# Performance work log

Hardware: AMD Instinct MI355X
Metric: run time of the kernel (lower is better)

The kernel has to match this reference:

```python
import jax, jax.numpy as jnp
import numpy as np

N = 50000   # nodes
E = 800000  # edges
H = 128     # hidden dim
V = 50000   # feats_per_node (embedding vocab)


def setup_inputs() -> dict:
    key = jax.random.key(0)
    ks = jax.random.split(key, 16)
    s = 0.05  # keep activations in a sane range
    return {
        "node_ids": jax.random.randint(ks[0], (N,), 0, V),
        "src": jax.random.randint(ks[1], (E,), 0, N),
        "dst": jnp.sort(jax.random.randint(ks[2], (E,), 0, N)),
        "emb": jax.random.normal(ks[3], (V, H), jnp.float32) * s,
        "W_pool1": jax.random.normal(ks[4], (H, H), jnp.float32) * s,
        "b_pool1": jax.random.normal(ks[5], (H,), jnp.float32) * s,
        "W_self1": jax.random.normal(ks[6], (H, H), jnp.float32) * s,
        "W_neigh1": jax.random.normal(ks[7], (H, H), jnp.float32) * s,
        "b1": jax.random.normal(ks[8], (H,), jnp.float32) * s,
        "W_pool2": jax.random.normal(ks[9], (H, H), jnp.float32) * s,
        "b_pool2": jax.random.normal(ks[10], (H,), jnp.float32) * s,
        "W_self2": jax.random.normal(ks[11], (H, H), jnp.float32) * s,
        "W_neigh2": jax.random.normal(ks[12], (H, H), jnp.float32) * s,
        "b2": jax.random.normal(ks[13], (H,), jnp.float32) * s,
    }


def _sage_pool_layer(h, src, dst, W_pool, b_pool, W_self, W_neigh, b):
    # DGL SAGEConv('pool'): per-src MLP, gather over edges, segmented max per dst.
    m = jax.nn.relu(h @ W_pool + b_pool)              # [N, H]
    msgs = m[src]                                     # [E, H] gather
    agg = jax.ops.segment_max(msgs, dst, num_segments=N,
                              indices_are_sorted=True)  # [N, H]
    agg = jnp.where(jnp.isneginf(agg), 0.0, agg)      # zero-in-degree -> 0 (DGL semantics)
    return h @ W_self + agg @ W_neigh + b


def reference(node_ids, src, dst, emb,
              W_pool1, b_pool1, W_self1, W_neigh1, b1,
              W_pool2, b_pool2, W_self2, W_neigh2, b2):
    h = emb[node_ids]                                 # embedding_h on 1-hot indices
    h = _sage_pool_layer(h, src, dst, W_pool1, b_pool1, W_self1, W_neigh1, b1)
    h = _sage_pool_layer(h, src, dst, W_pool2, b_pool2, W_self2, W_neigh2, b2)
    return h
```

## Files before the change

### kernel.cpp

```cpp
#include <hip/hip_runtime.h>

#define HD 128

typedef __attribute__((ext_vector_type(8))) short short8;
typedef __attribute__((ext_vector_type(4))) float floatx4;

typedef unsigned short ushort_t;
typedef unsigned int uint_t;

__device__ __forceinline__ ushort_t f2b(float f) {
    union { float f; uint_t u; } v; v.f = f;
    uint_t r = v.u + 0x7fff + ((v.u >> 16) & 1);
    return (ushort_t)(r >> 16);
}
__device__ __forceinline__ float b_lo(uint_t p) {
    union { uint_t u; float f; } v; v.u = p << 16; return v.f;
}
__device__ __forceinline__ float b_hi(uint_t p) {
    union { uint_t u; float f; } v; v.u = p & 0xffff0000u; return v.f;
}
__device__ __forceinline__ uint_t packb(float a, float b) {
    union { float f; uint_t u; } x, y; x.f = a; y.f = b;
    return (x.u >> 16) | (y.u & 0xffff0000u);
}

__global__ __launch_bounds__(256) void k_prep(const int* __restrict__ dst, int E,
                                              int* __restrict__ rp, int N,
                                              const int* __restrict__ ids,
                                              const float* __restrict__ emb,
                                              ushort_t* __restrict__ h0,
                                              const float* W0, const float* W1,
                                              const float* W2, const float* W3,
                                              const float* W4, const float* W5,
                                              ushort_t* __restrict__ Wpk,
                                              int nbG, int nbR) {
    int b = blockIdx.x;
    if (b < nbG) {
        int idx = b * 256 + threadIdx.x;
        int row = idx >> 5;
        if (row >= N) return;
        int c = (idx & 31) * 4;
        float4 v = *(const float4*)&emb[(size_t)ids[row] * HD + c];
        uint2 o;
        o.x = (uint_t)f2b(v.x) | ((uint_t)f2b(v.y) << 16);
        o.y = (uint_t)f2b(v.z) | ((uint_t)f2b(v.w) << 16);
        *(uint2*)&h0[(size_t)row * HD + c] = o;
    } else if (b < nbG + nbR) {
        int i = (b - nbG) * 256 + threadIdx.x;
        if (i > N) return;
        int lo = 0, hi = E;
        while (lo < hi) {
            int mid = (lo + hi) >> 1;
            if (dst[mid] < i) lo = mid + 1; else hi = mid;
        }
        rp[i] = lo;
    } else {
        int bb = b - nbG - nbR;
        const float* Ws[6] = {W0, W1, W2, W3, W4, W5};
        int mat = bb >> 6;
        int o = ((bb & 63) << 8) + threadIdx.x;
        int j = o & 7, l = (o >> 3) & 63, s = (o >> 9) & 3, t = o >> 11;
        int k = s * 32 + ((l >> 4) & 3) * 8 + j;
        int n = t * 16 + (l & 15);
        Wpk[(size_t)mat * 16384 + o] = f2b(Ws[mat][k * HD + n]);
    }
}

__global__ __launch_bounds__(256) void k_pool_mfma(const ushort_t* __restrict__ h,
                                                   const ushort_t* __restrict__ Wpk,
                                                   const float* __restrict__ bias,
                                                   ushort_t* __restrict__ m, int N) {
    int wave = blockIdx.x * 4 + (threadIdx.x >> 6);
    int row0 = wave * 32;
    if (row0 >= N) return;
    int l = threadIdx.x & 63;
    int ar0 = row0 + (l & 15); if (ar0 >= N) ar0 = N - 1;
    int ar1 = ar0 + 16;        if (ar1 >= N) ar1 = N - 1;
    int ac = (l >> 4) * 8;
    short8 a0[4], a1[4];
#pragma unroll
    for (int s = 0; s < 4; ++s) {
        a0[s] = *(const short8*)&h[(size_t)ar0 * HD + s * 32 + ac];
        a1[s] = *(const short8*)&h[(size_t)ar1 * HD + s * 32 + ac];
    }
    int rb = row0 + (l >> 4) * 4;
#pragma unroll
    for (int t = 0; t < 8; ++t) {
        floatx4 acc0 = {0.f, 0.f, 0.f, 0.f};
        floatx4 acc1 = {0.f, 0.f, 0.f, 0.f};
#pragma unroll
        for (int s = 0; s < 4; ++s) {
            short8 b = *(const short8*)&Wpk[(t * 4 + s) * 512 + l * 8];
            acc0 = __builtin_amdgcn_mfma_f32_16x16x32_bf16(a0[s], b, acc0, 0, 0, 0);
            acc1 = __builtin_amdgcn_mfma_f32_16x16x32_bf16(a1[s], b, acc1, 0, 0, 0);
        }
        int col = t * 16 + (l & 15);
        float bv = bias[col];
#pragma unroll
        for (int r = 0; r < 4; ++r) {
            int g0 = rb + r, g1 = rb + 16 + r;
            if (g0 < N) m[(size_t)g0 * HD + col] = f2b(fmaxf(acc0[r] + bv, 0.f));
            if (g1 < N) m[(size_t)g1 * HD + col] = f2b(fmaxf(acc1[r] + bv, 0.f));
        }
    }
}

template <bool F32OUT>
__global__ __launch_bounds__(256) void k_dual_mfma(const ushort_t* __restrict__ h,
                                                   const ushort_t* __restrict__ agg,
                                                   const ushort_t* __restrict__ WsPk,
                                                   const ushort_t* __restrict__ WnPk,
                                                   const float* __restrict__ bias,
                                                   void* __restrict__ outp, int N) {
    int wave = blockIdx.x * 4 + (threadIdx.x >> 6);
    int row0 = wave * 32;
    if (row0 >= N) return;
    int l = threadIdx.x & 63;
    int ar0 = row0 + (l & 15); if (ar0 >= N) ar0 = N - 1;
    int ar1 = ar0 + 16;        if (ar1 >= N) ar1 = N - 1;
    int ac = (l >> 4) * 8;
    short8 ah0[4], ah1[4], ag0[4], ag1[4];
#pragma unroll
    for (int s = 0; s < 4; ++s) {
        ah0[s] = *(const short8*)&h[(size_t)ar0 * HD + s * 32 + ac];
        ah1[s] = *(const short8*)&h[(size_t)ar1 * HD + s * 32 + ac];
        ag0[s] = *(const short8*)&agg[(size_t)ar0 * HD + s * 32 + ac];
        ag1[s] = *(const short8*)&agg[(size_t)ar1 * HD + s * 32 + ac];
    }
    int rb = row0 + (l >> 4) * 4;
#pragma unroll
    for (int t = 0; t < 8; ++t) {
        floatx4 acc0 = {0.f, 0.f, 0.f, 0.f};
        floatx4 acc1 = {0.f, 0.f, 0.f, 0.f};
#pragma unroll
        for (int s = 0; s < 4; ++s) {
            short8 bs = *(const short8*)&WsPk[(t * 4 + s) * 512 + l * 8];
            acc0 = __builtin_amdgcn_mfma_f32_16x16x32_bf16(ah0[s], bs, acc0, 0, 0, 0);
            acc1 = __builtin_amdgcn_mfma_f32_16x16x32_bf16(ah1[s], bs, acc1, 0, 0, 0);
        }
#pragma unroll
        for (int s = 0; s < 4; ++s) {
            short8 bn = *(const short8*)&WnPk[(t * 4 + s) * 512 + l * 8];
            acc0 = __builtin_amdgcn_mfma_f32_16x16x32_bf16(ag0[s], bn, acc0, 0, 0, 0);
            acc1 = __builtin_amdgcn_mfma_f32_16x16x32_bf16(ag1[s], bn, acc1, 0, 0, 0);
        }
        int col = t * 16 + (l & 15);
        float bv = bias[col];
#pragma unroll
        for (int r = 0; r < 4; ++r) {
            int g0 = rb + r, g1 = rb + 16 + r;
            float v0 = acc0[r] + bv, v1 = acc1[r] + bv;
            if (F32OUT) {
                if (g0 < N) ((float*)outp)[(size_t)g0 * HD + col] = v0;
                if (g1 < N) ((float*)outp)[(size_t)g1 * HD + col] = v1;
            } else {
                if (g0 < N) ((ushort_t*)outp)[(size_t)g0 * HD + col] = f2b(v0);
                if (g1 < N) ((ushort_t*)outp)[(size_t)g1 * HD + col] = f2b(v1);
            }
        }
    }
}

__global__ __launch_bounds__(256) void k_segmax(const ushort_t* __restrict__ m,
                                                const int* __restrict__ src,
                                                const int* __restrict__ rp,
                                                ushort_t* __restrict__ agg, int N) {
    int node = blockIdx.x * 8 + (threadIdx.x >> 5);
    if (node >= N) return;
    int lane = threadIdx.x & 31;
    int beg = rp[node], end = rp[node + 1];
    float a0 = 0.f, a1 = 0.f, a2 = 0.f, a3 = 0.f;
    float c0 = 0.f, c1 = 0.f, c2 = 0.f, c3 = 0.f;
    int e = beg;
    int e4 = beg + ((end - beg) & ~3);
    for (; e < e4; e += 4) {
        int s0 = src[e], s1 = src[e + 1], s2 = src[e + 2], s3 = src[e + 3];
        uint2 p0 = *(const uint2*)&m[(size_t)s0 * HD + lane * 4];
        uint2 p1 = *(const uint2*)&m[(size_t)s1 * HD + lane * 4];
        uint2 p2 = *(const uint2*)&m[(size_t)s2 * HD + lane * 4];
        uint2 p3 = *(const uint2*)&m[(size_t)s3 * HD + lane * 4];
        a0 = fmaxf(a0, b_lo(p0.x)); a1 = fmaxf(a1, b_hi(p0.x));
        a2 = fmaxf(a2, b_lo(p0.y)); a3 = fmaxf(a3, b_hi(p0.y));
        c0 = fmaxf(c0, b_lo(p1.x)); c1 = fmaxf(c1, b_hi(p1.x));
        c2 = fmaxf(c2, b_lo(p1.y)); c3 = fmaxf(c3, b_hi(p1.y));
        a0 = fmaxf(a0, b_lo(p2.x)); a1 = fmaxf(a1, b_hi(p2.x));
        a2 = fmaxf(a2, b_lo(p2.y)); a3 = fmaxf(a3, b_hi(p2.y));
        c0 = fmaxf(c0, b_lo(p3.x)); c1 = fmaxf(c1, b_hi(p3.x));
        c2 = fmaxf(c2, b_lo(p3.y)); c3 = fmaxf(c3, b_hi(p3.y));
    }
    for (; e < end; ++e) {
        uint2 p = *(const uint2*)&m[(size_t)src[e] * HD + lane * 4];
        a0 = fmaxf(a0, b_lo(p.x)); a1 = fmaxf(a1, b_hi(p.x));
        a2 = fmaxf(a2, b_lo(p.y)); a3 = fmaxf(a3, b_hi(p.y));
    }
    a0 = fmaxf(a0, c0); a1 = fmaxf(a1, c1); a2 = fmaxf(a2, c2); a3 = fmaxf(a3, c3);
    uint2 o; o.x = packb(a0, a1); o.y = packb(a2, a3);
    *(uint2*)&agg[(size_t)node * HD + lane * 4] = o;
}

extern "C" void kernel_launch(void* const* d_in, const int* in_sizes, int n_in,
                              void* d_out, int out_size, void* d_ws, size_t ws_size,
                              hipStream_t stream) {
    const int*   node_ids = (const int*)d_in[0];
    const int*   src      = (const int*)d_in[1];
    const int*   dst      = (const int*)d_in[2];
    const float* emb      = (const float*)d_in[3];
    const float* Wp1      = (const float*)d_in[4];
    const float* bp1      = (const float*)d_in[5];
    const float* Ws1      = (const float*)d_in[6];
    const float* Wn1      = (const float*)d_in[7];
    const float* b1       = (const float*)d_in[8];
    const float* Wp2      = (const float*)d_in[9];
    const float* bp2      = (const float*)d_in[10];
    const float* Ws2      = (const float*)d_in[11];
    const float* Wn2      = (const float*)d_in[12];
    const float* b2       = (const float*)d_in[13];
    float* out = (float*)d_out;

    const int N = in_sizes[0];
    const int E = in_sizes[1];

    char* ws = (char*)d_ws;
    int* rp = (int*)ws;
    size_t off = (((size_t)(N + 1) * 4) + 255) & ~(size_t)255;
    ushort_t* Wpk  = (ushort_t*)(ws + off);
    ushort_t* h0   = Wpk + 6 * 16384;
    ushort_t* bufM = h0 + (size_t)N * HD;
    ushort_t* bufA = bufM + (size_t)N * HD;
    ushort_t* h1   = bufA + (size_t)N * HD;

    const int nbG = (N * 32 + 255) / 256;
    const int nbR = (N + 1 + 255) / 256;
    const int nbP = 6 * 64;
    const int nb_gemm = (N + 127) / 128;
    const int nb_seg  = (N + 7) / 8;

    k_prep<<<nbG + nbR + nbP, 256, 0, stream>>>(dst, E, rp, N, node_ids, emb, h0,
                                                Wp1, Ws1, Wn1, Wp2, Ws2, Wn2, Wpk,
                                                nbG, nbR);

    const ushort_t* Wp1k = Wpk;
    const ushort_t* Ws1k = Wpk + 16384;
    const ushort_t* Wn1k = Wpk + 2 * 16384;
    const ushort_t* Wp2k = Wpk + 3 * 16384;
    const ushort_t* Ws2k = Wpk + 4 * 16384;
    const ushort_t* Wn2k = Wpk + 5 * 16384;

    k_pool_mfma<<<nb_gemm, 256, 0, stream>>>(h0, Wp1k, bp1, bufM, N);
    k_segmax<<<nb_seg, 256, 0, stream>>>(bufM, src, rp, bufA, N);
    k_dual_mfma<false><<<nb_gemm, 256, 0, stream>>>(h0, bufA, Ws1k, Wn1k, b1, h1, N);

    k_pool_mfma<<<nb_gemm, 256, 0, stream>>>(h1, Wp2k, bp2, bufM, N);
    k_segmax<<<nb_seg, 256, 0, stream>>>(bufM, src, rp, bufA, N);
    k_dual_mfma<true><<<nb_gemm, 256, 0, stream>>>(h1, bufA, Ws2k, Wn2k, b2, out, N);
}
```

Before: 245.9 us.

## Fuse embedding gather into first pool GEMM, stage weights in LDS, widen segmax

The embedding gather and bf16 conversion move out of the prep kernel and into the first pool GEMM, which writes h0 as a side output. All GEMM kernels now copy their packed weights into shared memory once per block instead of reading them from global memory on every wave. Segmax now assigns a full 64-lane wave per node, with the two half-waves taking alternate edges and merging through a cross-lane shuffle. The price is 32-64 KB of LDS per GEMM block, which may lower occupancy, plus extra staging work in every block.

```diff
diff --git a/kernel.cpp b/kernel.cpp
--- a/kernel.cpp
+++ b/kernel.cpp
@@ -23,30 +23,23 @@
     union { float f; uint_t u; } x, y; x.f = a; y.f = b;
     return (x.u >> 16) | (y.u & 0xffff0000u);
 }
+__device__ __forceinline__ short8 cvt8(const float* __restrict__ p) {
+    float4 u = *(const float4*)p, v = *(const float4*)(p + 4);
+    short8 r;
+    r[0] = (short)f2b(u.x); r[1] = (short)f2b(u.y); r[2] = (short)f2b(u.z); r[3] = (short)f2b(u.w);
+    r[4] = (short)f2b(v.x); r[5] = (short)f2b(v.y); r[6] = (short)f2b(v.z); r[7] = (short)f2b(v.w);
+    return r;
+}
 
 __global__ __launch_bounds__(256) void k_prep(const int* __restrict__ dst, int E,
                                               int* __restrict__ rp, int N,
-                                              const int* __restrict__ ids,
-                                              const float* __restrict__ emb,
-                                              ushort_t* __restrict__ h0,
                                               const float* W0, const float* W1,
                                               const float* W2, const float* W3,
                                               const float* W4, const float* W5,
-                                              ushort_t* __restrict__ Wpk,
-                                              int nbG, int nbR) {
+                                              ushort_t* __restrict__ Wpk, int nbR) {
     int b = blockIdx.x;
-    if (b < nbG) {
-        int idx = b * 256 + threadIdx.x;
-        int row = idx >> 5;
-        if (row >= N) return;
-        int c = (idx & 31) * 4;
-        float4 v = *(const float4*)&emb[(size_t)ids[row] * HD + c];
-        uint2 o;
-        o.x = (uint_t)f2b(v.x) | ((uint_t)f2b(v.y) << 16);
-        o.y = (uint_t)f2b(v.z) | ((uint_t)f2b(v.w) << 16);
-        *(uint2*)&h0[(size_t)row * HD + c] = o;
-    } else if (b < nbG + nbR) {
-        int i = (b - nbG) * 256 + threadIdx.x;
+    if (b < nbR) {
+        int i = b * 256 + threadIdx.x;
         if (i > N) return;
         int lo = 0, hi = E;
         while (lo < hi) {
@@ -55,7 +48,7 @@
         }
         rp[i] = lo;
     } else {
-        int bb = b - nbG - nbR;
+        int bb = b - nbR;
         const float* Ws[6] = {W0, W1, W2, W3, W4, W5};
         int mat = bb >> 6;
         int o = ((bb & 63) << 8) + threadIdx.x;
@@ -66,10 +59,71 @@
     }
 }
 
-__global__ __launch_bounds__(256) void k_pool_mfma(const ushort_t* __restrict__ h,
-                                                   const ushort_t* __restrict__ Wpk,
-                                                   const float* __restrict__ bias,
-                                                   ushort_t* __restrict__ m, int N) {
+__device__ __forceinline__ void stage_w(const ushort_t* __restrict__ g,
+                                        ushort_t* l, int tid) {
+#pragma unroll
+    for (int i = 0; i < 8; ++i) {
+        int off = i * 2048 + tid * 8;
+        *(short8*)&l[off] = *(const short8*)&g[off];
+    }
+}
+
+__global__ __launch_bounds__(256) void k_gather_pool(const int* __restrict__ ids,
+                                                     const float* __restrict__ emb,
+                                                     const ushort_t* __restrict__ Wpk,
+                                                     const float* __restrict__ bias,
+                                                     ushort_t* __restrict__ h0,
+                                                     ushort_t* __restrict__ m, int N) {
+    __shared__ ushort_t Wl[16384];
+    stage_w(Wpk, Wl, threadIdx.x);
+    __syncthreads();
+
+    int wave = blockIdx.x * 4 + (threadIdx.x >> 6);
+    int row0 = wave * 32;
+    if (row0 >= N) return;
+    int l = threadIdx.x & 63;
+    int ar0 = row0 + (l & 15); if (ar0 >= N) ar0 = N - 1;
+    int ar1 = ar0 + 16;        if (ar1 >= N) ar1 = N - 1;
+    int ac = (l >> 4) * 8;
+    int id0 = ids[ar0], id1 = ids[ar1];
+    short8 a0[4], a1[4];
+#pragma unroll
+    for (int s = 0; s < 4; ++s) {
+        a0[s] = cvt8(&emb[(size_t)id0 * HD + s * 32 + ac]);
+        a1[s] = cvt8(&emb[(size_t)id1 * HD + s * 32 + ac]);
+        *(short8*)&h0[(size_t)ar0 * HD + s * 32 + ac] = a0[s];
+        *(short8*)&h0[(size_t)ar1 * HD + s * 32 + ac] = a1[s];
+    }
+    int rb = row0 + (l >> 4) * 4;
+#pragma unroll
+    for (int t = 0; t < 8; ++t) {
+        floatx4 acc0 = {0.f, 0.f, 0.f, 0.f};
+        floatx4 acc1 = {0.f, 0.f, 0.f, 0.f};
+#pragma unroll
+        for (int s = 0; s < 4; ++s) {
+            short8 b = *(const short8*)&Wl[(t * 4 + s) * 512 + l * 8];
+            acc0 = __builtin_amdgcn_mfma_f32_16x16x32_bf16(a0[s], b, acc0, 0, 0, 0);
+            acc1 = __builtin_amdgcn_mfma_f32_16x16x32_bf16(a1[s], b, acc1, 0, 0, 0);
+        }
+        int col = t * 16 + (l & 15);
+        float bv = bias[col];
+#pragma unroll
+        for (int r = 0; r < 4; ++r) {
+            int g0 = rb + r, g1 = rb + 16 + r;
+            if (g0 < N) m[(size_t)g0 * HD + col] = f2b(fmaxf(acc0[r] + bv, 0.f));
+            if (g1 < N) m[(size_t)g1 * HD + col] = f2b(fmaxf(acc1[r] + bv, 0.f));
+        }
+    }
+}
+
+__global__ __launch_bounds__(256) void k_pool(const ushort_t* __restrict__ h,
+                                              const ushort_t* __restrict__ Wpk,
+                                              const float* __restrict__ bias,
+                                              ushort_t* __restrict__ m, int N) {
+    __shared__ ushort_t Wl[16384];
+    stage_w(Wpk, Wl, threadIdx.x);
+    __syncthreads();
+
     int wave = blockIdx.x * 4 + (threadIdx.x >> 6);
     int row0 = wave * 32;
     if (row0 >= N) return;
@@ -90,7 +144,7 @@
         floatx4 acc1 = {0.f, 0.f, 0.f, 0.f};
 #pragma unroll
         for (int s = 0; s < 4; ++s) {
-            short8 b = *(const short8*)&Wpk[(t * 4 + s) * 512 + l * 8];
+            short8 b = *(const short8*)&Wl[(t * 4 + s) * 512 + l * 8];
             acc0 = __builtin_amdgcn_mfma_f32_16x16x32_bf16(a0[s], b, acc0, 0, 0, 0);
             acc1 = __builtin_amdgcn_mfma_f32_16x16x32_bf16(a1[s], b, acc1, 0, 0, 0);
         }
@@ -105,13 +159,63 @@
     }
 }
 
+__global__ __launch_bounds__(256) void k_segmax(const ushort_t* __restrict__ m,
+                                                const int* __restrict__ src,
+                                                const int* __restrict__ rp,
+                                                ushort_t* __restrict__ agg, int N) {
+    int node = blockIdx.x * 4 + (threadIdx.x >> 6);
+    if (node >= N) return;
+    int l = threadIdx.x & 63;
+    int half = l >> 5;
+    int col4 = (l & 31) * 4;
+    int beg = rp[node], end = rp[node + 1];
+    float a0 = 0.f, a1 = 0.f, a2 = 0.f, a3 = 0.f;
+    float c0 = 0.f, c1 = 0.f, c2 = 0.f, c3 = 0.f;
+    int e = beg;
+    for (; e + 8 <= end; e += 8) {
+        int e0 = e + half, e1 = e + 2 + half, e2 = e + 4 + half, e3 = e + 6 + half;
+        uint2 p0 = *(const uint2*)&m[(size_t)src[e0] * HD + col4];
+        uint2 p1 = *(const uint2*)&m[(size_t)src[e1] * HD + col4];
+        uint2 p2 = *(const uint2*)&m[(size_t)src[e2] * HD + col4];
+        uint2 p3 = *(const uint2*)&m[(size_t)src[e3] * HD + col4];
+        a0 = fmaxf(a0, b_lo(p0.x)); a1 = fmaxf(a1, b_hi(p0.x));
+        a2 = fmaxf(a2, b_lo(p0.y)); a3 = fmaxf(a3, b_hi(p0.y));
+        c0 = fmaxf(c0, b_lo(p1.x)); c1 = fmaxf(c1, b_hi(p1.x));
+        c2 = fmaxf(c2, b_lo(p1.y)); c3 = fmaxf(c3, b_hi(p1.y));
+        a0 = fmaxf(a0, b_lo(p2.x)); a1 = fmaxf(a1, b_hi(p2.x));
+        a2 = fmaxf(a2, b_lo(p2.y)); a3 = fmaxf(a3, b_hi(p2.y));
+        c0 = fmaxf(c0, b_lo(p3.x)); c1 = fmaxf(c1, b_hi(p3.x));
+        c2 = fmaxf(c2, b_lo(p3.y)); c3 = fmaxf(c3, b_hi(p3.y));
+    }
+    for (; e < end; e += 2) {
+        int ee = e + half; if (ee >= end) ee = end - 1;
+        uint2 p = *(const uint2*)&m[(size_t)src[ee] * HD + col4];
+        a0 = fmaxf(a0, b_lo(p.x)); a1 = fmaxf(a1, b_hi(p.x));
+        a2 = fmaxf(a2, b_lo(p.y)); a3 = fmaxf(a3, b_hi(p.y));
+    }
+    a0 = fmaxf(a0, c0); a1 = fmaxf(a1, c1); a2 = fmaxf(a2, c2); a3 = fmaxf(a3, c3);
+    a0 = fmaxf(a0, __shfl_xor(a0, 32));
+    a1 = fmaxf(a1, __shfl_xor(a1, 32));
+    a2 = fmaxf(a2, __shfl_xor(a2, 32));
+    a3 = fmaxf(a3, __shfl_xor(a3, 32));
+    if (half == 0) {
+        uint2 o; o.x = packb(a0, a1); o.y = packb(a2, a3);
+        *(uint2*)&agg[(size_t)node * HD + col4] = o;
+    }
+}
+
 template <bool F32OUT>
-__global__ __launch_bounds__(256) void k_dual_mfma(const ushort_t* __restrict__ h,
-                                                   const ushort_t* __restrict__ agg,
-                                                   const ushort_t* __restrict__ WsPk,
-                                                   const ushort_t* __restrict__ WnPk,
-                                                   const float* __restrict__ bias,
-                                                   void* __restrict__ outp, int N) {
+__global__ __launch_bounds__(256) void k_dual(const ushort_t* __restrict__ h,
+                                              const ushort_t* __restrict__ agg,
+                                              const ushort_t* __restrict__ WsPk,
+                                              const ushort_t* __restrict__ WnPk,
+                                              const float* __restrict__ bias,
+                                              void* __restrict__ outp, int N) {
+    __shared__ ushort_t Wl[32768];
+    stage_w(WsPk, Wl, threadIdx.x);
+    stage_w(WnPk, Wl + 16384, threadIdx.x);
+    __syncthreads();
+
     int wave = blockIdx.x * 4 + (threadIdx.x >> 6);
     int row0 = wave * 32;
     if (row0 >= N) return;
@@ -134,13 +238,13 @@
         floatx4 acc1 = {0.f, 0.f, 0.f, 0.f};
 #pragma unroll
         for (int s = 0; s < 4; ++s) {
-            short8 bs = *(const short8*)&WsPk[(t * 4 + s) * 512 + l * 8];
+            short8 bs = *(const short8*)&Wl[(t * 4 + s) * 512 + l * 8];
             acc0 = __builtin_amdgcn_mfma_f32_16x16x32_bf16(ah0[s], bs, acc0, 0, 0, 0);
             acc1 = __builtin_amdgcn_mfma_f32_16x16x32_bf16(ah1[s], bs, acc1, 0, 0, 0);
         }
 #pragma unroll
         for (int s = 0; s < 4; ++s) {
-            short8 bn = *(const short8*)&WnPk[(t * 4 + s) * 512 + l * 8];
+            short8 bn = *(const short8*)&Wl[16384 + (t * 4 + s) * 512 + l * 8];
             acc0 = __builtin_amdgcn_mfma_f32_16x16x32_bf16(ag0[s], bn, acc0, 0, 0, 0);
             acc1 = __builtin_amdgcn_mfma_f32_16x16x32_bf16(ag1[s], bn, acc1, 0, 0, 0);
         }
@@ -159,43 +263,6 @@
             }
         }
     }
-}
-
-__global__ __launch_bounds__(256) void k_segmax(const ushort_t* __restrict__ m,
-                                                const int* __restrict__ src,
-                                                const int* __restrict__ rp,
-                                                ushort_t* __restrict__ agg, int N) {
-    int node = blockIdx.x * 8 + (threadIdx.x >> 5);
-    if (node >= N) return;
-    int lane = threadIdx.x & 31;
-    int beg = rp[node], end = rp[node + 1];
-    float a0 = 0.f, a1 = 0.f, a2 = 0.f, a3 = 0.f;
-    float c0 = 0.f, c1 = 0.f, c2 = 0.f, c3 = 0.f;
-    int e = beg;
-    int e4 = beg + ((end - beg) & ~3);
-    for (; e < e4; e += 4) {
-        int s0 = src[e], s1 = src[e + 1], s2 = src[e + 2], s3 = src[e + 3];
-        uint2 p0 = *(const uint2*)&m[(size_t)s0 * HD + lane * 4];
-        uint2 p1 = *(const uint2*)&m[(size_t)s1 * HD + lane * 4];
-        uint2 p2 = *(const uint2*)&m[(size_t)s2 * HD + lane * 4];
-        uint2 p3 = *(const uint2*)&m[(size_t)s3 * HD + lane * 4];
-        a0 = fmaxf(a0, b_lo(p0.x)); a1 = fmaxf(a1, b_hi(p0.x));
-        a2 = fmaxf(a2, b_lo(p0.y)); a3 = fmaxf(a3, b_hi(p0.y));
-        c0 = fmaxf(c0, b_lo(p1.x)); c1 = fmaxf(c1, b_hi(p1.x));
-        c2 = fmaxf(c2, b_lo(p1.y)); c3 = fmaxf(c3, b_hi(p1.y));
-        a0 = fmaxf(a0, b_lo(p2.x)); a1 = fmaxf(a1, b_hi(p2.x));
-        a2 = fmaxf(a2, b_lo(p2.y)); a3 = fmaxf(a3, b_hi(p2.y));
-        c0 = fmaxf(c0, b_lo(p3.x)); c1 = fmaxf(c1, b_hi(p3.x));
-        c2 = fmaxf(c2, b_lo(p3.y)); c3 = fmaxf(c3, b_hi(p3.y));
-    }
-    for (; e < end; ++e) {
-        uint2 p = *(const uint2*)&m[(size_t)src[e] * HD + lane * 4];
-        a0 = fmaxf(a0, b_lo(p.x)); a1 = fmaxf(a1, b_hi(p.x));
-        a2 = fmaxf(a2, b_lo(p.y)); a3 = fmaxf(a3, b_hi(p.y));
-    }
-    a0 = fmaxf(a0, c0); a1 = fmaxf(a1, c1); a2 = fmaxf(a2, c2); a3 = fmaxf(a3, c3);
-    uint2 o; o.x = packb(a0, a1); o.y = packb(a2, a3);
-    *(uint2*)&agg[(size_t)node * HD + lane * 4] = o;
 }
 
 extern "C" void kernel_launch(void* const* d_in, const int* in_sizes, int n_in,
@@ -225,19 +292,17 @@
     size_t off = (((size_t)(N + 1) * 4) + 255) & ~(size_t)255;
     ushort_t* Wpk  = (ushort_t*)(ws + off);
     ushort_t* h0   = Wpk + 6 * 16384;
-    ushort_t* bufM = h0 + (size_t)N * HD;
+    ushort_t* h1   = h0 + (size_t)N * HD;
+    ushort_t* bufM = h1 + (size_t)N * HD;
     ushort_t* bufA = bufM + (size_t)N * HD;
-    ushort_t* h1   = bufA + (size_t)N * HD;
-
-    const int nbG = (N * 32 + 255) / 256;
+
     const int nbR = (N + 1 + 255) / 256;
     const int nbP = 6 * 64;
     const int nb_gemm = (N + 127) / 128;
-    const int nb_seg  = (N + 7) / 8;
-
-    k_prep<<<nbG + nbR + nbP, 256, 0, stream>>>(dst, E, rp, N, node_ids, emb, h0,
-                                                Wp1, Ws1, Wn1, Wp2, Ws2, Wn2, Wpk,
-                                                nbG, nbR);
+    const int nb_seg  = (N + 3) / 4;
+
+    k_prep<<<nbR + nbP, 256, 0, stream>>>(dst, E, rp, N,
+                                          Wp1, Ws1, Wn1, Wp2, Ws2, Wn2, Wpk, nbR);
 
     const ushort_t* Wp1k = Wpk;
     const ushort_t* Ws1k = Wpk + 16384;
@@ -246,11 +311,10 @@
     const ushort_t* Ws2k = Wpk + 4 * 16384;
     const ushort_t* Wn2k = Wpk + 5 * 16384;
 
-    k_pool_mfma<<<nb_gemm, 256, 0, stream>>>(h0, Wp1k, bp1, bufM, N);
+    k_gather_pool<<<nb_gemm, 256, 0, stream>>>(node_ids, emb, Wp1k, bp1, h0, bufM, N);
     k_segmax<<<nb_seg, 256, 0, stream>>>(bufM, src, rp, bufA, N);
-    k_dual_mfma<false><<<nb_gemm, 256, 0, stream>>>(h0, bufA, Ws1k, Wn1k, b1, h1, N);
-
-    k_pool_mfma<<<nb_gemm, 256, 0, stream>>>(h1, Wp2k, bp2, bufM, N);
+    k_dual<false><<<nb_gemm, 256, 0, stream>>>(h0, bufA, Ws1k, Wn1k, b1, h1, N);
+    k_pool<<<nb_gemm, 256, 0, stream>>>(h1, Wp2k, bp2, bufM, N);
     k_segmax<<<nb_seg, 256, 0, stream>>>(bufM, src, rp, bufA, N);
-    k_dual_mfma<true><<<nb_gemm, 256, 0, stream>>>(h1, bufA, Ws2k, Wn2k, b2, out, N);
-}
+    k_dual<true><<<nb_gemm, 256, 0, stream>>>(h1, bufA, Ws2k, Wn2k, b2, out, N);
+}
```

Result: faster. 236.7 us (-3.7%).
